# Kernel tuning notes

Hardware: AMD Instinct MI355X
Metric: run time of the kernel (lower is better)

## Reference

```python
import jax, jax.numpy as jnp
import numpy as np

SQ3, SQ5, SQ15 = 3.0**0.5, 5.0**0.5, 15.0**0.5
M0, M1, M2 = 128, 64, 32
DIM = M0 + 3*M1 + 5*M2  # 480
N_GRAPHS, ATOMS_PER, N_BLOCKS = 512, 16, 8
N_NODES = N_GRAPHS * ATOMS_PER
N_EDGES = 100000
CUTOFF = 5.0
AVG_DEGREE = 15.57
AVG_NUM_NODES = 18.03
ATOM_MAP = np.array([-1, 0, -1, -1, -1, -1, 1, 2, 3, 4], dtype=np.int32)


def _sph(u):
    # component-normalized real spherical harmonics l=1,2 of unit vectors u [E,3]
    x, y, z = u[:, 0], u[:, 1], u[:, 2]
    sh1 = SQ3 * u
    sh2 = jnp.stack([SQ15*x*y, SQ15*y*z, 0.5*SQ5*(3.0*z*z - 1.0),
                     SQ15*x*z, 0.5*SQ15*(x*x - y*y)], axis=-1)
    return sh1, sh2


def _seg_softmax(logits, seg, n):
    m = jax.ops.segment_max(logits, seg, num_segments=n)
    e = jnp.exp(logits - m[seg])
    s = jax.ops.segment_sum(e, seg, num_segments=n)
    return e / (s[seg] + 1e-9)


def _energy(pos, fp, node_atom, edge_src, edge_dst, batch):
    (atom_table, rbf_centers, rbf_width, deg_W1, deg_W2, deg_W3,
     blk_Wv0, blk_Wv1, blk_Wv2, blk_Ws0, blk_Ws1, blk_Ws2,
     blk_rW1, blk_rW2, blk_rW3, blk_Wa_src, blk_Wa_dst, blk_Wa_e, blk_wa,
     blk_ff1, blk_ff2, blk_fg1, blk_fg2, blk_fW1, blk_fW2,
     ln_g, ln_b, head_W0, head_out) = fp
    N = pos.shape[0]
    mapped = jnp.asarray(ATOM_MAP)[node_atom]
    f0 = atom_table[mapped]                       # [N,128] scalar channels
    f1 = jnp.zeros((N, M1, 3), f0.dtype)
    f2 = jnp.zeros((N, M2, 5), f0.dtype)

    vec = pos[edge_src] - pos[edge_dst]           # [E,3]
    r = jnp.sqrt(jnp.sum(vec*vec, axis=1) + 1e-12)
    u = vec / r[:, None]
    sh1, sh2 = _sph(u)
    rbf = jnp.exp(-0.5 * ((r[:, None] - rbf_centers[None, :]) / rbf_width[None, :])**2)  # [E,128]

    # edge-degree embedding: radial-weighted SH scattered to dst, scaled by avg degree
    h = jax.nn.silu(rbf @ deg_W1)
    h = jax.nn.silu(h @ deg_W2)
    g = h @ deg_W3                                 # [E,224]
    g0, g1, g2 = g[:, :M0], g[:, M0:M0+M1], g[:, M0+M1:]
    inv = 1.0 / (AVG_DEGREE ** 0.5)
    f0 = f0 + inv * jax.ops.segment_sum(g0, edge_dst, num_segments=N)
    f1 = f1 + inv * jax.ops.segment_sum(g1[:, :, None]*sh1[:, None, :], edge_dst, num_segments=N)
    f2 = f2 + inv * jax.ops.segment_sum(g2[:, :, None]*sh2[:, None, :], edge_dst, num_segments=N)

    for i in range(N_BLOCKS):
        s0, s1, s2 = f0[edge_src], f1[edge_src], f2[edge_src]
        h = jax.nn.silu(rbf @ blk_rW1[i])
        h = jax.nn.silu(h @ blk_rW2[i])
        g = h @ blk_rW3[i]
        g0, g1, g2 = g[:, :M0], g[:, M0:M0+M1], g[:, M0+M1:]
        # equivariant tensor-product messages: value path (radial-gated) + SH-injection path
        m0 = (s0 @ blk_Wv0[i]) * g0 + s0 @ blk_Ws0[i]
        m1 = jnp.einsum('ecx,cd->edx', s1, blk_Wv1[i]) * g1[:, :, None] \
             + (s0 @ blk_Ws1[i])[:, :, None] * sh1[:, None, :]
        m2 = jnp.einsum('ecx,cd->edx', s2, blk_Wv2[i]) * g2[:, :, None] \
             + (s0 @ blk_Ws2[i])[:, :, None] * sh2[:, None, :]
        # scalar attention, softmax over incoming edges per destination node
        z = jnp.tanh(s0 @ blk_Wa_src[i] + f0[edge_dst] @ blk_Wa_dst[i] + h @ blk_Wa_e[i])
        a = _seg_softmax(z @ blk_wa[i], edge_dst, N)  # [E]
        f0 = f0 + jax.ops.segment_sum(a[:, None]*m0, edge_dst, num_segments=N)
        f1 = f1 + jax.ops.segment_sum(a[:, None, None]*m1, edge_dst, num_segments=N)
        f2 = f2 + jax.ops.segment_sum(a[:, None, None]*m2, edge_dst, num_segments=N)
        # equivariant FFN: scalar MLP + scalar-gated per-l channel mixing
        f0 = f0 + jax.nn.silu(f0 @ blk_ff1[i]) @ blk_ff2[i]
        f1 = f1 + jnp.einsum('ncx,cd->ndx', f1, blk_fW1[i]) * jax.nn.sigmoid(f0 @ blk_fg1[i])[:, :, None]
        f2 = f2 + jnp.einsum('ncx,cd->ndx', f2, blk_fW2[i]) * jax.nn.sigmoid(f0 @ blk_fg2[i])[:, :, None]

    flat = jnp.concatenate([f0, f1.reshape(N, 3*M1), f2.reshape(N, 5*M2)], axis=1)  # [N,480]
    mu = jnp.mean(flat, axis=1, keepdims=True)
    var = jnp.var(flat, axis=1, keepdims=True)
    flat = (flat - mu) * jax.lax.rsqrt(var + 1e-5) * ln_g + ln_b
    # head: only the 0e part can reach the final 1x0e output (equivariance)
    e_node = jax.nn.silu(flat[:, :M0] @ head_W0) @ head_out  # [N,1]
    energy = jax.ops.segment_sum(e_node[:, 0], batch, num_segments=N_GRAPHS) / (AVG_NUM_NODES ** 0.5)
    return energy  # [B]


def setup_inputs() -> dict:
    key = jax.random.key(0)
    rng = np.random.default_rng(0)
    B, A = N_GRAPHS, ATOMS_PER
    pos_np = rng.uniform(0.0, 6.0, size=(B, A, 3)).astype(np.float32)
    d = np.linalg.norm(pos_np[:, :, None, :] - pos_np[:, None, :, :], axis=-1)
    mask = (d < CUTOFF) & (d > 1e-6)
    gi, si, di = np.nonzero(mask)
    src = np.resize((gi*A + si).astype(np.int32), N_EDGES)
    dst = np.resize((gi*A + di).astype(np.int32), N_EDGES)
    atoms = rng.choice(np.array([1, 6, 7, 8, 9], dtype=np.int32), size=B*A)
    batch = np.repeat(np.arange(B, dtype=np.int32), A)

    ks = iter(jax.random.split(key, 40))
    def W(shape, fan):
        return jax.random.normal(next(ks), shape, jnp.float32) / np.sqrt(fan)
    D3 = M0 + M1 + M2  # 224
    return dict(
        pos=jnp.asarray(pos_np.reshape(B*A, 3)),
        atom_table=W((5, M0), 1.0),
        rbf_centers=jnp.linspace(0.0, CUTOFF, 128),
        rbf_width=jnp.full((128,), 0.25, jnp.float32),
        deg_W1=W((128, 64), 128), deg_W2=W((64, 64), 64), deg_W3=W((64, D3), 64),
        blk_Wv0=W((8, M0, M0), M0), blk_Wv1=W((8, M1, M1), M1), blk_Wv2=W((8, M2, M2), M2),
        blk_Ws0=W((8, M0, M0), M0), blk_Ws1=W((8, M0, M1), M0), blk_Ws2=W((8, M0, M2), M0),
        blk_rW1=W((8, 128, 64), 128), blk_rW2=W((8, 64, 64), 64), blk_rW3=W((8, 64, D3), 64),
        blk_Wa_src=W((8, M0, 32), M0), blk_Wa_dst=W((8, M0, 32), M0), blk_Wa_e=W((8, 64, 32), 64),
        blk_wa=W((8, 32), 32),
        blk_ff1=W((8, M0, 4*M0), M0), blk_ff2=W((8, 4*M0, M0), 4*M0),
        blk_fg1=W((8, M0, M1), M0), blk_fg2=W((8, M0, M2), M0),
        blk_fW1=W((8, M1, M1), M1), blk_fW2=W((8, M2, M2), M2),
        ln_g=jnp.ones((DIM,), jnp.float32), ln_b=jnp.zeros((DIM,), jnp.float32),
        head_W0=W((M0, M0), M0), head_out=W((M0, 1), M0),
        node_atom=jnp.asarray(atoms), edge_src=jnp.asarray(src),
        edge_dst=jnp.asarray(dst), batch=jnp.asarray(batch),
    )


def reference(pos, atom_table, rbf_centers, rbf_width, deg_W1, deg_W2, deg_W3,
              blk_Wv0, blk_Wv1, blk_Wv2, blk_Ws0, blk_Ws1, blk_Ws2,
              blk_rW1, blk_rW2, blk_rW3, blk_Wa_src, blk_Wa_dst, blk_Wa_e, blk_wa,
              blk_ff1, blk_ff2, blk_fg1, blk_fg2, blk_fW1, blk_fW2,
              ln_g, ln_b, head_W0, head_out,
              node_atom, edge_src, edge_dst, batch):
    fp = (atom_table, rbf_centers, rbf_width, deg_W1, deg_W2, deg_W3,
          blk_Wv0, blk_Wv1, blk_Wv2, blk_Ws0, blk_Ws1, blk_Ws2,
          blk_rW1, blk_rW2, blk_rW3, blk_Wa_src, blk_Wa_dst, blk_Wa_e, blk_wa,
          blk_ff1, blk_ff2, blk_fg1, blk_fg2, blk_fW1, blk_fW2,
          ln_g, ln_b, head_W0, head_out)

    def _tot(p):
        e = _energy(p, fp, node_atom, edge_src, edge_dst, batch)
        return jnp.sum(e), e

    (_, energy), gpos = jax.value_and_grad(_tot, has_aux=True)(pos)
    forces = -gpos  # dy = -dE/dpos, as in the torch autograd.grad call
    return energy, forces
```

## Files before the change

### kernel.cpp

```cpp
#include <hip/hip_runtime.h>
#include <string.h>
#include <math.h>

#define NE 100000
#define NN 8192
#define NG 512
#define CHF 25000
#define NF 4
#define CHB 20000
#define NB 5
#define CHIF 50000
#define NIF 2
#define CHIB 34000
#define NIB 3
#define NNC 8192

#define SQ3F  1.7320508075688772f
#define SQ5F  2.23606797749979f
#define SQ15F 3.872983346207417f

__constant__ int c_amap[10] = {-1,0,-1,-1,-1,-1,1,2,3,4};

typedef __attribute__((ext_vector_type(4))) float f32x4;
typedef __attribute__((ext_vector_type(8))) short bf16x8;
// ... 51 lines not shown
__global__ void k_mkedge(const int* perm, const int* src, const int* dst, int* src2, int* dst2){
  int k = blockIdx.x*256 + threadIdx.x;
  if (k < NE){ int e = perm[k]; src2[k] = src[e]; dst2[k] = dst[e]; }
}

__global__ void k_wcat(const float* Wv0,const float* Ws0,const float* Ws1,const float* Ws2, float* W){
  int t = blockIdx.x*256 + threadIdx.x;
  if (t >= 8*128*352) return;
  int i = t/45056, r = t - i*45056;
  int k = r/352, n = r - k*352;
  float v;
  if (n < 128) v = Wv0[(size_t)i*16384 + k*128 + n];
  else if (n < 256) v = Ws0[(size_t)i*16384 + k*128 + (n-128)];
  else if (n < 320) v = Ws1[(size_t)i*8192 + k*64 + (n-256)];
  else v = Ws2[(size_t)i*4096 + k*32 + (n-320)];
  W[t] = v;
}

template<int MT, bool TB, bool ACC, int ACT, bool GATHER, bool SPLIT, bool ARBF, bool DMUL, bool PREOUT>
__global__ __launch_bounds__(256) void k_mgemm(
    const float* __restrict__ A, const int* __restrict__ idx,
    const float* __restrict__ B, float* __restrict__ C,
    int M, int Nd, int K,
    const float* __restrict__ cen, const float* __restrict__ wid,
    const float* __restrict__ dm, float* __restrict__ pre)
{
  constexpr int TPR = 256/MT;
  constexpr int EPT = 32/TPR;
  constexpr int RT  = MT/16;
  __shared__ unsigned short Asb[(SPLIT?2:1)*MT*40];
// ... 65 lines not shown
        if (row >= M) continue;
        size_t o = (size_t)row*Nd + col;
        float x = acc[r][v];
        if (ACC) x += C[o];
        if (DMUL) x *= dsiluf(dm[o]);
        if (PREOUT) pre[o] = x;
        if (ACT == 1) x = siluf(x);
        else if (ACT == 2) x = tanhf(x);
        else if (ACT == 3) x = sigf(x);
        C[o] = x;
      }
    }
  }
}

template<int CI, int CO, int X, bool TB, bool ACC, bool GATHER, bool SPLIT>
__global__ __launch_bounds__(256) void k_meinsum(
    const float* __restrict__ A, const int* __restrict__ idx,
    const float* __restrict__ W, float* __restrict__ C, int M)
{
  __shared__ unsigned short Asb[(SPLIT?2:1)*2560];
  __shared__ unsigned short Btb[(SPLIT?2:1)*2560];
  const int bm = blockIdx.x*64;
  const int tid = threadIdx.x, wave = tid>>6, lane = tid&63;
  const int srow = tid>>2, soff = (tid&3)*8;
  f32x4 acc[4];
  #pragma unroll
  for (int r=0;r<4;r++) acc[r] = (f32x4){0.f,0.f,0.f,0.f};
  long abase = -1;
  {
    int grow = bm + srow;
    if (grow < M*X){
      int ge = grow / X, gx = grow - ge*X;
      int ar = GATHER ? idx[ge] : ge;
// ... 33 lines not shown
      }
    }
    __syncthreads();
  }
  int col = wave*16 + (lane&15);
  if (col < CO){
    #pragma unroll
    for (int r=0;r<4;r++){
      #pragma unroll
      for (int v=0;v<4;v++){
        int row = bm + r*16 + (lane>>4)*4 + v;
        if (row >= M*X) continue;
        int ge = row / X, gx = row - ge*X;
        size_t o = (size_t)ge*CO*X + (size_t)col*X + gx;
        float xx = acc[r][v];
        if (ACC) xx += C[o];
        C[o] = xx;
      }
    }
  }
}

__global__ void k_sentinel(float* o, int n, float v){
  int i = blockIdx.x*256 + threadIdx.x;
  if (i < n) o[i] = v;
}

__global__ void k_geom(const float* __restrict__ pos, const int* __restrict__ src, const int* __restrict__ dst,
                       float* __restrict__ U, float* __restrict__ Rr, float* __restrict__ SH2b){
  int e = blockIdx.x*256 + threadIdx.x;
  if (e >= NE) return;
  int s = src[e], d = dst[e];
// ... 7 lines not shown
  SH2b[e*5+0]=SQ15F*ux*uy;
  SH2b[e*5+1]=SQ15F*uy*uz;
  SH2b[e*5+2]=0.5f*SQ5F*(3.0f*uz*uz-1.0f);
  SH2b[e*5+3]=SQ15F*ux*uz;
  SH2b[e*5+4]=0.5f*SQ15F*(ux*ux-uy*uy);
}

__global__ void k_f0init(const int* __restrict__ na, const float* __restrict__ at, float* __restrict__ f0){
  int t = blockIdx.x*256 + threadIdx.x;
  if (t >= NN*128) return;
  int n = t>>7, j = t&127;
  int m = c_amap[na[n]];
  f0[t] = at[m*128+j];
}

__global__ void k_lambda(const float* __restrict__ Z, const float* __restrict__ wa, float* __restrict__ P_c, int cnt){
  int e = blockIdx.x*256 + threadIdx.x;
  if (e >= cnt) return;
  float s = 0.0f;
  #pragma unroll
  for (int k=0;k<32;k++) s += Z[e*32+k]*wa[k];
  P_c[e] = expf(s);
}

__global__ void k_norm(const float* __restrict__ P, const float* __restrict__ S,
                       const int* __restrict__ dst, float* __restrict__ AB){
  int e = blockIdx.x*256 + threadIdx.x;
  if (e < NE) AB[e] = P[e]/(S[dst[e]]+1e-9f);
}

__global__ void k_finy(const float* __restrict__ x0,const float* __restrict__ x1,const float* __restrict__ x2,
                       float* __restrict__ y0,float* __restrict__ y1,float* __restrict__ y2,
                       const float* __restrict__ S){
  int t = blockIdx.x*256 + threadIdx.x;
  if (t >= NN*480) return;
  if (t < NN*128){ int n=t>>7; y0[t]=x0[t]+y0[t]/(S[n]+1e-9f); }
  else if (t < NN*320){ int q=t-NN*128; int n=q/192; y1[q]=x1[q]+y1[q]/(S[n]+1e-9f); }
  else { int q=t-NN*320; int n=q/160; y2[q]=x2[q]+y2[q]/(S[n]+1e-9f); }
}

__global__ void k_q3(const float* __restrict__ f0,const float* __restrict__ f1,const float* __restrict__ f2,
                     unsigned short* __restrict__ ck){
  int t = blockIdx.x*256 + threadIdx.x;
  if (t >= NN*480) return;
  float v;
  if (t < NN*128) v = f0[t];
  else if (t < NN*320) v = f1[t-NN*128];
  else v = f2[t-NN*320];
  ck[t] = f2b(v);
}
__global__ void k_dq3(const unsigned short* __restrict__ ck,
                      float* __restrict__ f0,float* __restrict__ f1,float* __restrict__ f2){
  int t = blockIdx.x*256 + threadIdx.x;
  if (t >= NN*480) return;
  float v = b2f(ck[t]);
  if (t < NN*128) f0[t]=v;
  else if (t < NN*320) f1[t-NN*128]=v;
  else f2[t-NN*320]=v;
}

template<bool INIT>
__global__ __launch_bounds__(512) void k_agg(
  float* __restrict__ f0o,float* __restrict__ f1o,float* __restrict__ f2o,
  const float* __restrict__ SC,const float* __restrict__ sv1,const float* __restrict__ sv2,
  const float* __restrict__ g,const float* __restrict__ U,const float* __restrict__ SH2b,
  const float* __restrict__ aArr,const int* __restrict__ keys,const int* __restrict__ dst,
  float* __restrict__ SACC, int c0, int c1)
{
  __shared__ float acc[7680];
  int b = blockIdx.x, lo = b<<4;
  int e0 = lbound(keys, NE, lo), e1 = lbound(keys, NE, lo+16);
  if (e0 < c0) e0 = c0;
  if (e1 > c1) e1 = c1;
// ... 171 lines not shown
      for (int x=0;x<5;x++) DSH2[e*5+x]+=c[x];
    }
    if (lane<32){
      float dsw=0.0f, dg2=0.0f;
      #pragma unroll
      for (int x=0;x<5;x++){ dsw+=dm[x]*SH2b[e*5+x]; dg2+=dm[x]*svo[x]; }
      SC[(size_t)el*352+320+lane]=dsw;
      DG[el*224+192+lane]=dg2;
      #pragma unroll
      for (int x=0;x<5;x++) SV2[el*160+lane*5+x]=dm[x]*g2;
    }
  }
}

template<int CD,int X>
__global__ void k_gatefwd(float* __restrict__ f, const float* __restrict__ V, const float* __restrict__ P){
  int t=blockIdx.x*256+threadIdx.x;
  const int ox=CD*X;
  if (t>=NN*ox) return;
  int n=t/ox, rem=t-n*ox, d=rem/X;
  f[t] += V[t]*P[n*CD+d];
}

template<int CD,int X>
__global__ void k_gateback(const float* __restrict__ dfB, float* __restrict__ V,
                           const float* __restrict__ P, float* __restrict__ DPa){
  int t=blockIdx.x*256+threadIdx.x;
  if (t>=NN*CD) return;
  float p=P[t];
  float dp=0.0f;
  #pragma unroll
  for (int x=0;x<X;x++){ dp += dfB[t*X+x]*V[t*X+x]; }
  #pragma unroll
  for (int x=0;x<X;x++){ V[t*X+x] = dfB[t*X+x]*p; }
  DPa[t] = dp*p*(1.0f-p);
}

__global__ __launch_bounds__(256) void k_dr(const float* __restrict__ DRBF, const float* __restrict__ Rr,
    const float* __restrict__ cen, const float* __restrict__ wid, float* __restrict__ DRa, int c0, int cnt){
  int w=threadIdx.x>>6, lane=threadIdx.x&63;
  int el=blockIdx.x*4+w;
  if (el>=cnt) return;
  int e=c0+el;
  float r=Rr[e], s=0.0f;
  for (int k=lane;k<128;k+=64){
    float c=cen[k], wd=wid[k];
    float t=(r-c)/wd;
    float rb=expf(-0.5f*t*t);
    s += DRBF[el*128+k]*rb*((c-r)/(wd*wd));
  }
// ... 120 lines not shown

__global__ void k_esum(const float* __restrict__ EN, float* __restrict__ out){
  int b=blockIdx.x*64+threadIdx.x;
  if (b<NG){
    float s=0.0f;
    for (int k=0;k<16;k++) s+=EN[b*16+k];
    out[b]=s;
  }
}

#define MG(MT,TB,ACC,ACT,GA,SP,AR,DM,PO, A,IDX,B,C,M,Nd,K, CEN,WID,DMp,POp) \
  k_mgemm<MT,TB,ACC,ACT,GA,SP,AR,DM,PO><<<dim3((unsigned)(((M)+(MT)-1)/(MT)),(unsigned)(((Nd)+63)/64)),dim3(256),0,stream>>>((A),(IDX),(B),(C),(M),(Nd),(K),(CEN),(WID),(DMp),(POp))
#define MGEMM(MT,TB,ACC,ACT,GA, A,IDX,B,C,M,Nd,K) MG(MT,TB,ACC,ACT,GA,false,false,false,false, A,IDX,B,C,M,Nd,K, nullptr,nullptr,nullptr,nullptr)
#define MGEMM3(MT,TB,ACC,ACT,GA, A,IDX,B,C,M,Nd,K) MG(MT,TB,ACC,ACT,GA,true,false,false,false, A,IDX,B,C,M,Nd,K, nullptr,nullptr,nullptr,nullptr)
#define MEINS(CI,CO,X,TB,ACC,GA, A,IDX,Wt,C,M) \
  k_meinsum<CI,CO,X,TB,ACC,GA,false><<<dim3((unsigned)(((M)*(X)+63)/64)),dim3(256),0,stream>>>((A),(IDX),(Wt),(C),(M))
#define MEINS3(CI,CO,X,TB,ACC,GA, A,IDX,Wt,C,M) \
  k_meinsum<CI,CO,X,TB,ACC,GA,true><<<dim3((unsigned)(((M)*(X)+63)/64)),dim3(256),0,stream>>>((A),(IDX),(Wt),(C),(M))
#define G256(n) dim3((unsigned)(((n)+255)/256)),dim3(256),0,stream
#define GW4(n) dim3((unsigned)(((n)+3)/4)),dim3(256),0,stream

extern "C" void kernel_launch(void* const* d_in, const int* in_sizes, int n_in,
                              void* d_out, int out_size, void* d_ws, size_t ws_size,
                              hipStream_t stream)
{
  const float* pos =(const float*)d_in[0];
  const float* atab=(const float*)d_in[1];
  const float* rbfc=(const float*)d_in[2];
  const float* rbfw=(const float*)d_in[3];
  const float* degW1=(const float*)d_in[4];
  const float* degW2=(const float*)d_in[5];
  const float* degW3=(const float*)d_in[6];
  const float* Wv0=(const float*)d_in[7];
// ... 27 lines not shown
  size_t off=0;
  auto al=[&](size_t n)->float*{ float* q=Wp+off; off+=n; return q; };

  const size_t SLOT = (size_t)NN*480;
  unsigned short* CKB = (unsigned short*)al((9*SLOT+1)/2);
  float* FA0=al((size_t)NN*128); float* FA1=al((size_t)NN*192); float* FA2=al((size_t)NN*160);
  float* FB0=al((size_t)NN*128); float* FB1=al((size_t)NN*192); float* FB2=al((size_t)NN*160);
  float* DI0=al((size_t)NN*128); float* DI1=al((size_t)NN*192); float* DI2=al((size_t)NN*160);
  float* DY0=al((size_t)NN*128); float* DY1=al((size_t)NN*192); float* DY2=al((size_t)NN*160);
  float* U=al((size_t)NE*3); float* Rr=al(NE); float* SH2b=al((size_t)NE*5);
  float* ABLK=al(8ULL*NE); float* LAM=al(NE);
  float* SSUM=al(NN); float* ENODE=al(NN); float* SACC=al(NN);
  float* DRr=al(NE); float* DSH1=al((size_t)NE*3); float* DSH2=al((size_t)NE*5);
  float* DPOS=al((size_t)NN*3);
  float* WCATF=al(8ULL*128*352);
  int* ROWS =(int*)al(NN+1);
  int* CNT  =(int*)al(NN);
  int* POSB =(int*)al(NN);
  int* PERMB=(int*)al(NE);
  int* ESRC2=(int*)al(NE);
  int* EDST2=(int*)al(NE);

  const size_t UNI = 28800000;
  float* UN = al(UNI);
  float* TBc=UN;
  float* DTc=TBc+(size_t)NNC*512;
  float* P1 =DTc+(size_t)NNC*512;
  float* P2 =P1 +(size_t)NN*64;
  float* V1 =P2 +(size_t)NN*32;
  float* V2 =V1 +(size_t)NN*192;
  float* DPb=V2 +(size_t)NN*160;
  float* F0N=DPb+(size_t)NN*64;

  float* outE=(float*)d_out;
  float* outF=outE+NG;

  if (off*sizeof(float) > ws_size){
    k_sentinel<<<G256(out_size)>>>(outE, out_size, (float)ws_size);
    return;
  }

  (void)hipMemsetAsync(CNT,0,NN*sizeof(int),stream);
  k_hist<<<G256(NE)>>>(edst,CNT,NE);
  k_scan0<<<dim3(1),dim3(256),0,stream>>>(CNT,ROWS);
  (void)hipMemcpyAsync(POSB,ROWS,NN*sizeof(int),hipMemcpyDeviceToDevice,stream);
  k_fillperm<<<G256(NE)>>>(edst,POSB,PERMB,NE);
  k_mkedge<<<G256(NE)>>>(PERMB,esrc,edst,ESRC2,EDST2);
  k_wcat<<<G256(8*128*352)>>>(Wv0,Ws0,Ws1,Ws2,WCATF);

  k_geom<<<G256(NE)>>>(pos,ESRC2,EDST2,U,Rr,SH2b);
  k_f0init<<<G256(NN*128)>>>(natom,atab,FA0);
  (void)hipMemsetAsync(FA1,0,(size_t)NN*192*4,stream);
  (void)hipMemsetAsync(FA2,0,(size_t)NN*160*4,stream);
  (void)hipMemsetAsync(DRr,0,(size_t)NE*4,stream);
  (void)hipMemsetAsync(DSH1,0,(size_t)NE*3*4,stream);
  (void)hipMemsetAsync(DSH2,0,(size_t)NE*5*4,stream);
  (void)hipMemsetAsync(DPOS,0,(size_t)NN*3*4,stream);

  {
    float* H1=UN; float* H2=H1+(size_t)CHIF*64; float* Gc=H2+(size_t)CHIF*64;
    for (int cc=0;cc<NIF;cc++){
      int c0e=cc*CHIF, cnt=(c0e+CHIF<=NE)?CHIF:(NE-c0e);
      MG(64,false,false,1,false, true,true,false,false, Rr+c0e,nullptr,degW1,H1, cnt,64,128, rbfc,rbfw,nullptr,nullptr);
      MGEMM3(64,false,false,1,false, H1,nullptr,degW2,H2, cnt,64,64);
      MGEMM3(64,false,false,0,false, H2,nullptr,degW3,Gc, cnt,224,64);
      k_agg<true><<<dim3(NG),dim3(512),0,stream>>>(FA0,FA1,FA2,
        nullptr,nullptr,nullptr, Gc,U,SH2b, nullptr, EDST2,EDST2, nullptr, c0e,c0e+cnt);
    }
// ... 1 lines not shown
  k_q3<<<G256(NN*480)>>>(FA0,FA1,FA2, CKB);

  float *c0_=FA0,*c1_=FA1,*c2_=FA2, *n0_=FB0,*n1_=FB1,*n2_=FB2;

  {
    float* H1  =UN;
    float* H2  =H1  +(size_t)CHF*64;
    float* Gc  =H2  +(size_t)CHF*64;
    float* SCAT=Gc  +(size_t)CHF*224;
    float* SV1 =SCAT+(size_t)CHF*352;
    float* SV2 =SV1 +(size_t)CHF*192;
    float* Zc  =SV2 +(size_t)CHF*160;
    for (int i=0;i<8;i++){
      const float* Wv1i=Wv1+(size_t)i*4096; const float* Wv2i=Wv2+(size_t)i*1024;
      const float* rW1i=rW1+(size_t)i*8192; const float* rW2i=rW2+(size_t)i*4096; const float* rW3i=rW3+(size_t)i*14336;
      const float* WaSi=WaS+(size_t)i*4096; const float* WaDi=WaD+(size_t)i*4096; const float* WaEi=WaE+(size_t)i*2048;
      const float* ff1i=ff1+(size_t)i*65536; const float* ff2i=ff2+(size_t)i*65536;
      const float* fg1i=fg1+(size_t)i*8192; const float* fg2i=fg2+(size_t)i*4096;
      const float* fW1i=fW1+(size_t)i*4096; const float* fW2i=fW2+(size_t)i*1024;
      const float* WCi=WCATF+(size_t)i*45056;
      float* AB=ABLK+(size_t)i*NE;

      (void)hipMemsetAsync(SACC,0,(size_t)NN*4,stream);
      (void)hipMemsetAsync(n0_,0,(size_t)NN*128*4,stream);
      (void)hipMemsetAsync(n1_,0,(size_t)NN*192*4,stream);
      (void)hipMemsetAsync(n2_,0,(size_t)NN*160*4,stream);
      for (int cc=0;cc<NF;cc++){
        int c0e=cc*CHF, cnt=(c0e+CHF<=NE)?CHF:(NE-c0e);
        MG(64,false,false,1,false, true,true,false,false, Rr+c0e,nullptr,rW1i,H1, cnt,64,128, rbfc,rbfw,nullptr,nullptr);
        MGEMM3(64,false,false,1,false, H1,nullptr,rW2i,H2, cnt,64,64);
        MGEMM3(64,false,false,0,false, H2,nullptr,rW3i,Gc, cnt,224,64);
        MGEMM3(64,false,false,0,true,  c0_,ESRC2+c0e,WaSi,Zc, cnt,32,128);
        MGEMM3(64,false,true, 0,true,  c0_,EDST2+c0e,WaDi,Zc, cnt,32,128);
        MGEMM3(64,false,true, 2,false, H2,nullptr,WaEi,Zc, cnt,32,64);
        k_lambda<<<G256(cnt)>>>(Zc, wab+(size_t)i*32, LAM+c0e, cnt);
        MGEMM3(64,false,false,0,true, c0_,ESRC2+c0e,WCi,SCAT, cnt,352,128);
        MEINS3(64,64,3,false,false,true, c1_,ESRC2+c0e,Wv1i,SV1, cnt);
        MEINS3(32,32,5,false,false,true, c2_,ESRC2+c0e,Wv2i,SV2, cnt);
        k_agg<false><<<dim3(NG),dim3(512),0,stream>>>(n0_,n1_,n2_,
          SCAT,SV1,SV2, Gc,U,SH2b, LAM, EDST2,EDST2, SACC, c0e,c0e+cnt);
      }
      k_norm<<<G256(NE)>>>(LAM,SACC,EDST2,AB);
      k_finy<<<G256(NN*480)>>>(c0_,c1_,c2_, n0_,n1_,n2_, SACC);
      k_q3<<<G256(NN*480)>>>(n0_,n1_,n2_, CKB+(size_t)(i+1)*SLOT);
      for (int nc=0;nc<NN/NNC;nc++){
        MGEMM3(64,false,false,1,false, n0_+(size_t)nc*NNC*128,nullptr,ff1i,TBc, NNC,512,128);
        MGEMM3(64,false,true, 0,false, TBc,nullptr,ff2i, n0_+(size_t)nc*NNC*128, NNC,128,512);
      }
      MGEMM3(32,false,false,3,false, n0_,nullptr,fg1i,P1, NN,64,128);
      MGEMM3(32,false,false,3,false, n0_,nullptr,fg2i,P2, NN,32,128);
      MEINS3(64,64,3,false,false,false, n1_,nullptr,fW1i,V1, NN);
      MEINS3(32,32,5,false,false,false, n2_,nullptr,fW2i,V2, NN);
      k_gatefwd<64,3><<<G256(NN*192)>>>(n1_,V1,P1);
      k_gatefwd<32,5><<<G256(NN*160)>>>(n2_,V2,P2);
      float* t;
      t=c0_;c0_=n0_;n0_=t; t=c1_;c1_=n1_;n1_=t; t=c2_;c2_=n2_;n2_=t;
    }
  }

  k_lnhead<<<dim3(NN),dim3(64),0,stream>>>(c0_,c1_,c2_, lng,lnb,W0h,hout, ENODE, DI0,DI1,DI2);
  k_esum<<<dim3(8),dim3(64),0,stream>>>(ENODE,outE);

  {
    float* PRE1=UN;
    float* PRE2=PRE1+(size_t)CHB*64;
    float* H1  =PRE2+(size_t)CHB*64;
    float* H2  =H1  +(size_t)CHB*64;
    float* Gc  =H2  +(size_t)CHB*64;
    float* DGc =Gc  +(size_t)CHB*224;
    float* SCAT=DGc +(size_t)CHB*224;
    float* SV1 =SCAT+(size_t)CHB*352;
    float* SV2 =SV1 +(size_t)CHB*192;
    float* Zc  =SV2 +(size_t)CHB*160;
    float* DE0 =PRE1;
    float* RBFc=DGc;
    float* DZD =Gc;
    for (int i=7;i>=0;--i){
      const float* Wv1i=Wv1+(size_t)i*4096; const float* Wv2i=Wv2+(size_t)i*1024;
      const float* rW1i=rW1+(size_t)i*8192; const float* rW2i=rW2+(size_t)i*4096; const float* rW3i=rW3+(size_t)i*14336;
      const float* WaSi=WaS+(size_t)i*4096; const float* WaDi=WaD+(size_t)i*4096; const float* WaEi=WaE+(size_t)i*2048;
      const float* ff1i=ff1+(size_t)i*65536; const float* ff2i=ff2+(size_t)i*65536;
      const float* fg1i=fg1+(size_t)i*8192; const float* fg2i=fg2+(size_t)i*4096;
      const float* fW1i=fW1+(size_t)i*4096; const float* fW2i=fW2+(size_t)i*1024;
      const float* WCi=WCATF+(size_t)i*45056;
      const float* AB=ABLK+(size_t)i*NE;

      k_dq3<<<G256(NN*480)>>>(CKB+(size_t)i*SLOT, FA0,FA1,FA2);
      if (i>0){
        const float* pf1=ff1+(size_t)(i-1)*65536; const float* pf2=ff2+(size_t)(i-1)*65536;
        const float* pg1=fg1+(size_t)(i-1)*8192; const float* pg2=fg2+(size_t)(i-1)*4096;
        const float* pW1=fW1+(size_t)(i-1)*4096; const float* pW2=fW2+(size_t)(i-1)*1024;
        for (int nc=0;nc<NN/NNC;nc++){
          MGEMM(64,false,false,1,false, FA0+(size_t)nc*NNC*128,nullptr,pf1,TBc, NNC,512,128);
          MGEMM(64,false,true, 0,false, TBc,nullptr,pf2, FA0+(size_t)nc*NNC*128, NNC,128,512);
        }
        MGEMM(32,false,false,3,false, FA0,nullptr,pg1,P1, NN,64,128);
        MGEMM(32,false,false,3,false, FA0,nullptr,pg2,P2, NN,32,128);
        MEINS(64,64,3,false,false,false, FA1,nullptr,pW1,V1, NN);
        MEINS(32,32,5,false,false,false, FA2,nullptr,pW2,V2, NN);
        k_gatefwd<64,3><<<G256(NN*192)>>>(FA1,V1,P1);
        k_gatefwd<32,5><<<G256(NN*160)>>>(FA2,V2,P2);
      }
      k_dq3<<<G256(NN*480)>>>(CKB+(size_t)(i+1)*SLOT, FB0,FB1,FB2);
      (void)hipMemcpyAsync(F0N,FB0,(size_t)NN*128*4,hipMemcpyDeviceToDevice,stream);
      for (int nc=0;nc<NN/NNC;nc++){
        MGEMM(64,false,false,1,false, FB0+(size_t)nc*NNC*128,nullptr,ff1i,TBc, NNC,512,128);
        MGEMM(64,false,true, 0,false, TBc,nullptr,ff2i, F0N+(size_t)nc*NNC*128, NNC,128,512);
      }
      MGEMM(32,false,false,3,false, F0N,nullptr,fg1i,P1, NN,64,128);
      MGEMM(32,false,false,3,false, F0N,nullptr,fg2i,P2, NN,32,128);
      MEINS(64,64,3,false,false,false, FB1,nullptr,fW1i,V1, NN);
      MEINS(32,32,5,false,false,false, FB2,nullptr,fW2i,V2, NN);
      k_gateback<64,3><<<G256(NN*64)>>>(DI1,V1,P1,DPb);
      MGEMM(64,true,true,0,false, DPb,nullptr,fg1i,DI0, NN,128,64);
      (void)hipMemcpyAsync(DY1,DI1,(size_t)NN*192*4,hipMemcpyDeviceToDevice,stream);
      MEINS(64,64,3,true,true,false, V1,nullptr,fW1i,DY1, NN);
      k_gateback<32,5><<<G256(NN*32)>>>(DI2,V2,P2,DPb);
      MGEMM(64,true,true,0,false, DPb,nullptr,fg2i,DI0, NN,128,32);
      (void)hipMemcpyAsync(DY2,DI2,(size_t)NN*160*4,hipMemcpyDeviceToDevice,stream);
      MEINS(32,32,5,true,true,false, V2,nullptr,fW2i,DY2, NN);
      (void)hipMemcpyAsync(DY0,DI0,(size_t)NN*128*4,hipMemcpyDeviceToDevice,stream);
      for (int nc=0;nc<NN/NNC;nc++){
        MGEMM(64,false,false,0,false, FB0+(size_t)nc*NNC*128,nullptr,ff1i,TBc, NNC,512,128);
        MG(64,true,false,0,false, false,false,true,false, DI0+(size_t)nc*NNC*128,nullptr,ff2i,DTc, NNC,512,128, nullptr,nullptr,TBc,nullptr);
        MGEMM(64,true,true,0,false, DTc,nullptr,ff1i, DY0+(size_t)nc*NNC*128, NNC,128,512);
      }
      k_ssum<<<dim3(NN/4),dim3(256),0,stream>>>(FA0,FA1,FA2,FB0,FB1,FB2,DY0,DY1,DY2,SSUM);
      (void)hipMemcpyAsync(DI0,DY0,(size_t)NN*128*4,hipMemcpyDeviceToDevice,stream);
      (void)hipMemcpyAsync(DI1,DY1,(size_t)NN*192*4,hipMemcpyDeviceToDevice,stream);
      (void)hipMemcpyAsync(DI2,DY2,(size_t)NN*160*4,hipMemcpyDeviceToDevice,stream);
      for (int cc=0;cc<NB;cc++){
        int c0e=cc*CHB, cnt=(c0e+CHB<=NE)?CHB:(NE-c0e);
        MG(64,false,false,1,false, false,true,false,true, Rr+c0e,nullptr,rW1i,H1, cnt,64,128, rbfc,rbfw,nullptr,PRE1);
        MG(64,false,false,1,false, false,false,false,true, H1,nullptr,rW2i,H2, cnt,64,64, nullptr,nullptr,nullptr,PRE2);
        MGEMM(64,false,false,0,false, H2,nullptr,rW3i,Gc, cnt,224,64);
        MGEMM(64,false,false,0,true,  FA0,ESRC2+c0e,WaSi,Zc, cnt,32,128);
        MGEMM(64,false,true, 0,true,  FA0,EDST2+c0e,WaDi,Zc, cnt,32,128);
        MGEMM(64,false,true, 2,false, H2,nullptr,WaEi,Zc, cnt,32,64);
        MGEMM(64,false,false,0,true, FA0,ESRC2+c0e,WCi,SCAT, cnt,352,128);
        MEINS(64,64,3,false,false,true, FA1,ESRC2+c0e,Wv1i,SV1, cnt);
        MEINS(32,32,5,false,false,true, FA2,ESRC2+c0e,Wv2i,SV2, cnt);
        k_bedge<<<GW4(cnt)>>>(SCAT,SV1,SV2, Gc,U,SH2b, DY0,DY1,DY2, EDST2, SSUM,
                              wab+(size_t)i*32, Zc, AB, DGc, DSH1, DSH2, c0e, cnt);
        MGEMM(64,true,false,0,false, Zc,nullptr,WaEi,H2, cnt,64,32);
        MG(64,true,true,0,false, false,false,true,false, DGc,nullptr,rW3i,H2, cnt,64,224, nullptr,nullptr,PRE2,nullptr);
        MG(64,true,false,0,false, false,false,true,false, H2,nullptr,rW2i,H1, cnt,64,64, nullptr,nullptr,PRE1,nullptr);
        MGEMM(64,true,false,0,false, H1,nullptr,rW1i,RBFc, cnt,128,64);
        k_dr<<<GW4(cnt)>>>(RBFc,Rr,rbfc,rbfw,DRr, c0e,cnt);
        MGEMM(64,true,false,0,false, SCAT,nullptr,WCi,DE0, cnt,128,352);
        MGEMM(64,true,true, 0,false, Zc,nullptr,WaSi,DE0, cnt,128,32);
        MGEMM(64,true,false,0,false, Zc,nullptr,WaDi,DZD, cnt,128,32);
        MEINS(64,64,3,true,false,false, SV1,nullptr,Wv1i,SV1, cnt);
        MEINS(32,32,5,true,false,false, SV2,nullptr,Wv2i,SV2, cnt);
        k_scat<<<dim3(NG),dim3(640),0,stream>>>(DI0,DI1,DI2, DE0,DZD,SV1,SV2, ESRC2,EDST2, c0e,c0e+cnt);
      }
    }
  }
// ... 27 lines not shown
```

Measured before the change: 32.96 ms.

## Fuse attention-logit GEMMs, gate GEMMs, and post-block elementwise kernels

Concatenates the src/dst/edge attention weights into one K=320 matrix so a single k_zgemm computes tanh logits and the exp(lambda) reduction in one pass. This replaces three GEMMs plus a lambda kernel, in both the forward and backward recompute. It also merges the two gate-weight GEMMs into one 96-wide GEMM and folds the gating update into the einsum epilogue. It further fuses the norm, finalize and quantize kernels, and the two dequantize kernels, into single launches. The intent is fewer launches and less intermediate memory traffic, at the cost of pointer-swapping bookkeeping between f1/f2 buffers, which could introduce aliasing mistakes.

```diff
diff --git a/kernel.cpp b/kernel.cpp
--- a/kernel.cpp
+++ b/kernel.cpp
@@ -89,6 +89,27 @@
   else if (n < 256) v = Ws0[(size_t)i*16384 + k*128 + (n-128)];
   else if (n < 320) v = Ws1[(size_t)i*8192 + k*64 + (n-256)];
   else v = Ws2[(size_t)i*4096 + k*32 + (n-320)];
+  W[t] = v;
+}
+__global__ void k_wcatz(const float* WaS,const float* WaD,const float* WaE, float* W){
+  int t = blockIdx.x*256 + threadIdx.x;
+  if (t >= 8*320*32) return;
+  int i = t/10240, r = t - i*10240;
+  int k = r/32, c = r - k*32;
+  float v;
+  if (k < 128) v = WaS[(size_t)i*4096 + k*32 + c];
+  else if (k < 256) v = WaD[(size_t)i*4096 + (k-128)*32 + c];
+  else v = WaE[(size_t)i*2048 + (k-256)*32 + c];
+  W[t] = v;
+}
+__global__ void k_wcatg(const float* fg1,const float* fg2, float* W){
+  int t = blockIdx.x*256 + threadIdx.x;
+  if (t >= 8*128*96) return;
+  int i = t/12288, r = t - i*12288;
+  int k = r/96, c = r - k*96;
+  float v;
+  if (c < 64) v = fg1[(size_t)i*8192 + k*64 + c];
+  else v = fg2[(size_t)i*4096 + k*32 + (c-64)];
   W[t] = v;
 }
 
@@ -184,10 +205,96 @@
   }
 }
 
-template<int CI, int CO, int X, bool TB, bool ACC, bool GATHER, bool SPLIT>
+template<bool SPLIT, bool LAMB>
+__global__ __launch_bounds__(256) void k_zgemm(
+    const float* __restrict__ F0, const int* __restrict__ sidx, const int* __restrict__ didx,
+    const float* __restrict__ H2v, const float* __restrict__ WZ, const float* __restrict__ wa,
+    float* __restrict__ Zc, float* __restrict__ LAM, int M)
+{
+  __shared__ unsigned short Asb[(SPLIT?2:1)*64*40];
+  __shared__ unsigned short Btb[(SPLIT?2:1)*2560];
+  __shared__ float lacc[128];
+  const int bm = blockIdx.x*64;
+  const int tid = threadIdx.x, wave = tid>>6, lane = tid&63;
+  const int arow_s = tid>>2, aoff = (tid&3)*8;
+  const int bsrow = tid>>2, bsoff = (tid&3)*8;
+  f32x4 acc[4];
+  #pragma unroll
+  for (int r=0;r<4;r++) acc[r] = (f32x4){0.f,0.f,0.f,0.f};
+  long sb=-1, db=-1, hb=-1;
+  {
+    int gr = bm + arow_s;
+    if (gr < M){ sb=(long)sidx[gr]*128; db=(long)didx[gr]*128; hb=(long)gr*64; }
+  }
+  for (int k0=0;k0<320;k0+=32){
+    long ab; int rk; const float* sp;
+    if (k0 < 128){ ab=sb; rk=k0; sp=F0; }
+    else if (k0 < 256){ ab=db; rk=k0-128; sp=F0; }
+    else { ab=hb; rk=k0-256; sp=H2v; }
+    #pragma unroll
+    for (int i=0;i<8;i++){
+      float v = (ab>=0) ? sp[ab + rk + aoff + i] : 0.0f;
+      unsigned short h = f2b(v);
+      Asb[arow_s*40 + aoff + i] = h;
+      if (SPLIT) Asb[64*40 + arow_s*40 + aoff + i] = f2b(v - b2f(h));
+    }
+    #pragma unroll
+    for (int i=0;i<8;i++){
+      int kk = k0 + bsoff + i;
+      float v = (bsrow < 32) ? WZ[kk*32 + bsrow] : 0.0f;
+      unsigned short h = f2b(v);
+      Btb[bsrow*40 + bsoff + i] = h;
+      if (SPLIT) Btb[2560 + bsrow*40 + bsoff + i] = f2b(v - b2f(h));
+    }
+    __syncthreads();
+    int boff = (wave*16 + (lane&15))*40 + (lane>>4)*8;
+    bf16x8 bh = *(const bf16x8*)&Btb[boff];
+    #pragma unroll
+    for (int r=0;r<4;r++){
+      int aoff2 = (r*16 + (lane&15))*40 + (lane>>4)*8;
+      bf16x8 ah = *(const bf16x8*)&Asb[aoff2];
+      acc[r] = __builtin_amdgcn_mfma_f32_16x16x32_bf16(ah, bh, acc[r], 0,0,0);
+      if (SPLIT){
+        bf16x8 bl = *(const bf16x8*)&Btb[2560 + boff];
+        bf16x8 al = *(const bf16x8*)&Asb[64*40 + aoff2];
+        acc[r] = __builtin_amdgcn_mfma_f32_16x16x32_bf16(ah, bl, acc[r], 0,0,0);
+        acc[r] = __builtin_amdgcn_mfma_f32_16x16x32_bf16(al, bh, acc[r], 0,0,0);
+      }
+    }
+    __syncthreads();
+  }
+  int col = wave*16 + (lane&15);
+  if (wave < 2){
+    #pragma unroll
+    for (int r=0;r<4;r++){
+      #pragma unroll
+      for (int v=0;v<4;v++){
+        int row = bm + r*16 + (lane>>4)*4 + v;
+        float z = tanhf(acc[r][v]);
+        if (row < M) Zc[(size_t)row*32 + col] = z;
+        if (LAMB){
+          float p = (row < M) ? z*wa[col] : 0.0f;
+          #pragma unroll
+          for (int o=8;o>0;o>>=1) p += __shfl_xor(p, o, 64);
+          if ((lane&15)==0) lacc[wave*64 + r*16 + (lane>>4)*4 + v] = p;
+        }
+      }
+    }
+  }
+  if (LAMB){
+    __syncthreads();
+    if (tid < 64){
+      int row = bm + tid;
+      if (row < M) LAM[row] = expf(lacc[tid] + lacc[64+tid]);
+    }
+  }
+}
+
+template<int CI, int CO, int X, bool TB, bool ACC, bool GATHER, bool SPLIT, bool GATE>
 __global__ __launch_bounds__(256) void k_meinsum(
     const float* __restrict__ A, const int* __restrict__ idx,
-    const float* __restrict__ W, float* __restrict__ C, int M)
+    const float* __restrict__ W, float* __restrict__ C, int M,
+    const float* __restrict__ P, int PS, int POFF)
 {
   __shared__ unsigned short Asb[(SPLIT?2:1)*2560];
   __shared__ unsigned short Btb[(SPLIT?2:1)*2560];
@@ -251,8 +358,13 @@
         int ge = row / X, gx = row - ge*X;
         size_t o = (size_t)ge*CO*X + (size_t)col*X + gx;
         float xx = acc[r][v];
-        if (ACC) xx += C[o];
-        C[o] = xx;
+        if (GATE){
+          float p = P[(size_t)ge*PS + POFF + col];
+          C[o] = A[o] + xx*p;
+        } else {
+          if (ACC) xx += C[o];
+          C[o] = xx;
+        }
       }
     }
   }
@@ -290,29 +402,18 @@
   f0[t] = at[m*128+j];
 }
 
-__global__ void k_lambda(const float* __restrict__ Z, const float* __restrict__ wa, float* __restrict__ P_c, int cnt){
-  int e = blockIdx.x*256 + threadIdx.x;
-  if (e >= cnt) return;
-  float s = 0.0f;
-  #pragma unroll
-  for (int k=0;k<32;k++) s += Z[e*32+k]*wa[k];
-  P_c[e] = expf(s);
-}
-
-__global__ void k_norm(const float* __restrict__ P, const float* __restrict__ S,
-                       const int* __restrict__ dst, float* __restrict__ AB){
-  int e = blockIdx.x*256 + threadIdx.x;
-  if (e < NE) AB[e] = P[e]/(S[dst[e]]+1e-9f);
-}
-
-__global__ void k_finy(const float* __restrict__ x0,const float* __restrict__ x1,const float* __restrict__ x2,
-                       float* __restrict__ y0,float* __restrict__ y1,float* __restrict__ y2,
-                       const float* __restrict__ S){
+__global__ void k_postblk(const float* __restrict__ x0,const float* __restrict__ x1,const float* __restrict__ x2,
+                          float* __restrict__ y0,float* __restrict__ y1,float* __restrict__ y2,
+                          const float* __restrict__ S, unsigned short* __restrict__ ck,
+                          const float* __restrict__ Pl, const int* __restrict__ dst, float* __restrict__ AB){
   int t = blockIdx.x*256 + threadIdx.x;
+  if (t < NE) AB[t] = Pl[t]/(S[dst[t]]+1e-9f);
   if (t >= NN*480) return;
-  if (t < NN*128){ int n=t>>7; y0[t]=x0[t]+y0[t]/(S[n]+1e-9f); }
-  else if (t < NN*320){ int q=t-NN*128; int n=q/192; y1[q]=x1[q]+y1[q]/(S[n]+1e-9f); }
-  else { int q=t-NN*320; int n=q/160; y2[q]=x2[q]+y2[q]/(S[n]+1e-9f); }
+  float v;
+  if (t < NN*128){ int n=t>>7; v = x0[t] + y0[t]/(S[n]+1e-9f); y0[t]=v; }
+  else if (t < NN*320){ int q=t-NN*128; int n=q/192; v = x1[q] + y1[q]/(S[n]+1e-9f); y1[q]=v; }
+  else { int q=t-NN*320; int n=q/160; v = x2[q] + y2[q]/(S[n]+1e-9f); y2[q]=v; }
+  ck[t] = f2b(v);
 }
 
 __global__ void k_q3(const float* __restrict__ f0,const float* __restrict__ f1,const float* __restrict__ f2,
@@ -325,14 +426,15 @@
   else v = f2[t-NN*320];
   ck[t] = f2b(v);
 }
-__global__ void k_dq3(const unsigned short* __restrict__ ck,
-                      float* __restrict__ f0,float* __restrict__ f1,float* __restrict__ f2){
+__global__ void k_dq3x2(const unsigned short* __restrict__ cka, const unsigned short* __restrict__ ckb,
+                        float* __restrict__ a0,float* __restrict__ a1,float* __restrict__ a2,
+                        float* __restrict__ b0,float* __restrict__ b1,float* __restrict__ b2){
   int t = blockIdx.x*256 + threadIdx.x;
   if (t >= NN*480) return;
-  float v = b2f(ck[t]);
-  if (t < NN*128) f0[t]=v;
-  else if (t < NN*320) f1[t-NN*128]=v;
-  else f2[t-NN*320]=v;
+  float va = b2f(cka[t]), vb = b2f(ckb[t]);
+  if (t < NN*128){ a0[t]=va; b0[t]=vb; }
+  else if (t < NN*320){ int q=t-NN*128; a1[q]=va; b1[q]=vb; }
+  else { int q=t-NN*320; a2[q]=va; b2[q]=vb; }
 }
 
 template<bool INIT>
@@ -534,26 +636,18 @@
 }
 
 template<int CD,int X>
-__global__ void k_gatefwd(float* __restrict__ f, const float* __restrict__ V, const float* __restrict__ P){
-  int t=blockIdx.x*256+threadIdx.x;
-  const int ox=CD*X;
-  if (t>=NN*ox) return;
-  int n=t/ox, rem=t-n*ox, d=rem/X;
-  f[t] += V[t]*P[n*CD+d];
-}
-
-template<int CD,int X>
 __global__ void k_gateback(const float* __restrict__ dfB, float* __restrict__ V,
-                           const float* __restrict__ P, float* __restrict__ DPa){
+                           const float* __restrict__ P12, float* __restrict__ DPa, int poff){
   int t=blockIdx.x*256+threadIdx.x;
   if (t>=NN*CD) return;
-  float p=P[t];
+  int n=t/CD, d=t-n*CD;
+  float p=P12[(size_t)n*96+poff+d];
   float dp=0.0f;
   #pragma unroll
-  for (int x=0;x<X;x++){ dp += dfB[t*X+x]*V[t*X+x]; }
+  for (int x=0;x<X;x++){ dp += dfB[(size_t)t*X+x]*V[(size_t)t*X+x]; }
   #pragma unroll
-  for (int x=0;x<X;x++){ V[t*X+x] = dfB[t*X+x]*p; }
-  DPa[t] = dp*p*(1.0f-p);
+  for (int x=0;x<X;x++){ V[(size_t)t*X+x] = dfB[(size_t)t*X+x]*p; }
+  DPa[(size_t)n*96+poff+d] = dp*p*(1.0f-p);
 }
 
 __global__ __launch_bounds__(256) void k_dr(const float* __restrict__ DRBF, const float* __restrict__ Rr,
@@ -704,9 +798,11 @@
 #define MGEMM(MT,TB,ACC,ACT,GA, A,IDX,B,C,M,Nd,K) MG(MT,TB,ACC,ACT,GA,false,false,false,false, A,IDX,B,C,M,Nd,K, nullptr,nullptr,nullptr,nullptr)
 #define MGEMM3(MT,TB,ACC,ACT,GA, A,IDX,B,C,M,Nd,K) MG(MT,TB,ACC,ACT,GA,true,false,false,false, A,IDX,B,C,M,Nd,K, nullptr,nullptr,nullptr,nullptr)
 #define MEINS(CI,CO,X,TB,ACC,GA, A,IDX,Wt,C,M) \
-  k_meinsum<CI,CO,X,TB,ACC,GA,false><<<dim3((unsigned)(((M)*(X)+63)/64)),dim3(256),0,stream>>>((A),(IDX),(Wt),(C),(M))
+  k_meinsum<CI,CO,X,TB,ACC,GA,false,false><<<dim3((unsigned)(((M)*(X)+63)/64)),dim3(256),0,stream>>>((A),(IDX),(Wt),(C),(M),nullptr,0,0)
 #define MEINS3(CI,CO,X,TB,ACC,GA, A,IDX,Wt,C,M) \
-  k_meinsum<CI,CO,X,TB,ACC,GA,true><<<dim3((unsigned)(((M)*(X)+63)/64)),dim3(256),0,stream>>>((A),(IDX),(Wt),(C),(M))
+  k_meinsum<CI,CO,X,TB,ACC,GA,true,false><<<dim3((unsigned)(((M)*(X)+63)/64)),dim3(256),0,stream>>>((A),(IDX),(Wt),(C),(M),nullptr,0,0)
+#define MEINSG(CI,CO,X,SP, A,Wt,C,M, Pp,POFF) \
+  k_meinsum<CI,CO,X,false,false,false,SP,true><<<dim3((unsigned)(((M)*(X)+63)/64)),dim3(256),0,stream>>>((A),nullptr,(Wt),(C),(M),(Pp),96,(POFF))
 #define G256(n) dim3((unsigned)(((n)+255)/256)),dim3(256),0,stream
 #define GW4(n) dim3((unsigned)(((n)+3)/4)),dim3(256),0,stream
 
@@ -764,6 +860,8 @@
   float* DRr=al(NE); float* DSH1=al((size_t)NE*3); float* DSH2=al((size_t)NE*5);
   float* DPOS=al((size_t)NN*3);
   float* WCATF=al(8ULL*128*352);
+  float* WCATZ=al(8ULL*320*32);
+  float* WCATG=al(8ULL*128*96);
   int* ROWS =(int*)al(NN+1);
   int* CNT  =(int*)al(NN);
   int* POSB =(int*)al(NN);
@@ -775,12 +873,11 @@
   float* UN = al(UNI);
   float* TBc=UN;
   float* DTc=TBc+(size_t)NNC*512;
-  float* P1 =DTc+(size_t)NNC*512;
-  float* P2 =P1 +(size_t)NN*64;
-  float* V1 =P2 +(size_t)NN*32;
+  float* P12=DTc+(size_t)NNC*512;
+  float* V1 =P12+(size_t)NN*96;
   float* V2 =V1 +(size_t)NN*192;
   float* DPb=V2 +(size_t)NN*160;
-  float* F0N=DPb+(size_t)NN*64;
+  float* F0N=DPb+(size_t)NN*96;
 
   float* outE=(float*)d_out;
   float* outF=outE+NG;
@@ -797,11 +894,12 @@
   k_fillperm<<<G256(NE)>>>(edst,POSB,PERMB,NE);
   k_mkedge<<<G256(NE)>>>(PERMB,esrc,edst,ESRC2,EDST2);
   k_wcat<<<G256(8*128*352)>>>(Wv0,Ws0,Ws1,Ws2,WCATF);
+  k_wcatz<<<G256(8*320*32)>>>(WaS,WaD,WaE,WCATZ);
+  k_wcatg<<<G256(8*128*96)>>>(fg1,fg2,WCATG);
 
   k_geom<<<G256(NE)>>>(pos,ESRC2,EDST2,U,Rr,SH2b);
   k_f0init<<<G256(NN*128)>>>(natom,atab,FA0);
-  (void)hipMemsetAsync(FA1,0,(size_t)NN*192*4,stream);
-  (void)hipMemsetAsync(FA2,0,(size_t)NN*160*4,stream);
+  (void)hipMemsetAsync(FA1,0,(size_t)NN*352*4,stream);
   (void)hipMemsetAsync(DRr,0,(size_t)NE*4,stream);
   (void)hipMemsetAsync(DSH1,0,(size_t)NE*3*4,stream);
   (void)hipMemsetAsync(DSH2,0,(size_t)NE*5*4,stream);
@@ -833,47 +931,39 @@
     for (int i=0;i<8;i++){
       const float* Wv1i=Wv1+(size_t)i*4096; const float* Wv2i=Wv2+(size_t)i*1024;
       const float* rW1i=rW1+(size_t)i*8192; const float* rW2i=rW2+(size_t)i*4096; const float* rW3i=rW3+(size_t)i*14336;
-      const float* WaSi=WaS+(size_t)i*4096; const float* WaDi=WaD+(size_t)i*4096; const float* WaEi=WaE+(size_t)i*2048;
+      const float* WZi=WCATZ+(size_t)i*10240;
       const float* ff1i=ff1+(size_t)i*65536; const float* ff2i=ff2+(size_t)i*65536;
-      const float* fg1i=fg1+(size_t)i*8192; const float* fg2i=fg2+(size_t)i*4096;
+      const float* fgCi=WCATG+(size_t)i*12288;
       const float* fW1i=fW1+(size_t)i*4096; const float* fW2i=fW2+(size_t)i*1024;
       const float* WCi=WCATF+(size_t)i*45056;
       float* AB=ABLK+(size_t)i*NE;
 
       (void)hipMemsetAsync(SACC,0,(size_t)NN*4,stream);
       (void)hipMemsetAsync(n0_,0,(size_t)NN*128*4,stream);
-      (void)hipMemsetAsync(n1_,0,(size_t)NN*192*4,stream);
-      (void)hipMemsetAsync(n2_,0,(size_t)NN*160*4,stream);
+      (void)hipMemsetAsync(n1_,0,(size_t)NN*352*4,stream);
       for (int cc=0;cc<NF;cc++){
         int c0e=cc*CHF, cnt=(c0e+CHF<=NE)?CHF:(NE-c0e);
         MG(64,false,false,1,false, true,true,false,false, Rr+c0e,nullptr,rW1i,H1, cnt,64,128, rbfc,rbfw,nullptr,nullptr);
         MGEMM3(64,false,false,1,false, H1,nullptr,rW2i,H2, cnt,64,64);
         MGEMM3(64,false,false,0,false, H2,nullptr,rW3i,Gc, cnt,224,64);
-        MGEMM3(64,false,false,0,true,  c0_,ESRC2+c0e,WaSi,Zc, cnt,32,128);
-        MGEMM3(64,false,true, 0,true,  c0_,EDST2+c0e,WaDi,Zc, cnt,32,128);
-        MGEMM3(64,false,true, 2,false, H2,nullptr,WaEi,Zc, cnt,32,64);
-        k_lambda<<<G256(cnt)>>>(Zc, wab+(size_t)i*32, LAM+c0e, cnt);
+        k_zgemm<true,true><<<dim3((unsigned)((cnt+63)/64)),dim3(256),0,stream>>>(
+            c0_, ESRC2+c0e, EDST2+c0e, H2, WZi, wab+(size_t)i*32, Zc, LAM+c0e, cnt);
         MGEMM3(64,false,false,0,true, c0_,ESRC2+c0e,WCi,SCAT, cnt,352,128);
         MEINS3(64,64,3,false,false,true, c1_,ESRC2+c0e,Wv1i,SV1, cnt);
         MEINS3(32,32,5,false,false,true, c2_,ESRC2+c0e,Wv2i,SV2, cnt);
         k_agg<false><<<dim3(NG),dim3(512),0,stream>>>(n0_,n1_,n2_,
           SCAT,SV1,SV2, Gc,U,SH2b, LAM, EDST2,EDST2, SACC, c0e,c0e+cnt);
       }
-      k_norm<<<G256(NE)>>>(LAM,SACC,EDST2,AB);
-      k_finy<<<G256(NN*480)>>>(c0_,c1_,c2_, n0_,n1_,n2_, SACC);
-      k_q3<<<G256(NN*480)>>>(n0_,n1_,n2_, CKB+(size_t)(i+1)*SLOT);
+      k_postblk<<<G256(NN*480)>>>(c0_,c1_,c2_, n0_,n1_,n2_, SACC, CKB+(size_t)(i+1)*SLOT, LAM, EDST2, AB);
       for (int nc=0;nc<NN/NNC;nc++){
         MGEMM3(64,false,false,1,false, n0_+(size_t)nc*NNC*128,nullptr,ff1i,TBc, NNC,512,128);
         MGEMM3(64,false,true, 0,false, TBc,nullptr,ff2i, n0_+(size_t)nc*NNC*128, NNC,128,512);
       }
-      MGEMM3(32,false,false,3,false, n0_,nullptr,fg1i,P1, NN,64,128);
-      MGEMM3(32,false,false,3,false, n0_,nullptr,fg2i,P2, NN,32,128);
-      MEINS3(64,64,3,false,false,false, n1_,nullptr,fW1i,V1, NN);
-      MEINS3(32,32,5,false,false,false, n2_,nullptr,fW2i,V2, NN);
-      k_gatefwd<64,3><<<G256(NN*192)>>>(n1_,V1,P1);
-      k_gatefwd<32,5><<<G256(NN*160)>>>(n2_,V2,P2);
+      MGEMM3(64,false,false,3,false, n0_,nullptr,fgCi,P12, NN,96,128);
+      MEINSG(64,64,3,true, n1_,fW1i,c1_, NN, P12, 0);
+      MEINSG(32,32,5,true, n2_,fW2i,c2_, NN, P12, 64);
       float* t;
-      t=c0_;c0_=n0_;n0_=t; t=c1_;c1_=n1_;n1_=t; t=c2_;c2_=n2_;n2_=t;
+      t=c0_;c0_=n0_;n0_=t;
     }
   }
 
@@ -897,69 +987,65 @@
     for (int i=7;i>=0;--i){
       const float* Wv1i=Wv1+(size_t)i*4096; const float* Wv2i=Wv2+(size_t)i*1024;
       const float* rW1i=rW1+(size_t)i*8192; const float* rW2i=rW2+(size_t)i*4096; const float* rW3i=rW3+(size_t)i*14336;
+      const float* WZi=WCATZ+(size_t)i*10240;
       const float* WaSi=WaS+(size_t)i*4096; const float* WaDi=WaD+(size_t)i*4096; const float* WaEi=WaE+(size_t)i*2048;
       const float* ff1i=ff1+(size_t)i*65536; const float* ff2i=ff2+(size_t)i*65536;
-      const float* fg1i=fg1+(size_t)i*8192; const float* fg2i=fg2+(size_t)i*4096;
+      const float* fgCi=WCATG+(size_t)i*12288;
       const float* fW1i=fW1+(size_t)i*4096; const float* fW2i=fW2+(size_t)i*1024;
       const float* WCi=WCATF+(size_t)i*45056;
       const float* AB=ABLK+(size_t)i*NE;
-
-      k_dq3<<<G256(NN*480)>>>(CKB+(size_t)i*SLOT, FA0,FA1,FA2);
+      float *fa1=FA1, *fa2=FA2, *dy1=DY1, *dy2=DY2;
+
+      k_dq3x2<<<G256(NN*480)>>>(CKB+(size_t)i*SLOT, CKB+(size_t)(i+1)*SLOT, FA0,FA1,FA2, FB0,FB1,FB2);
       if (i>0){
         const float* pf1=ff1+(size_t)(i-1)*65536; const float* pf2=ff2+(size_t)(i-1)*65536;
-        const float* pg1=fg1+(size_t)(i-1)*8192; const float* pg2=fg2+(size_t)(i-1)*4096;
+        const float* pgC=WCATG+(size_t)(i-1)*12288;
         const float* pW1=fW1+(size_t)(i-1)*4096; const float* pW2=fW2+(size_t)(i-1)*1024;
         for (int nc=0;nc<NN/NNC;nc++){
           MGEMM(64,false,false,1,false, FA0+(size_t)nc*NNC*128,nullptr,pf1,TBc, NNC,512,128);
           MGEMM(64,false,true, 0,false, TBc,nullptr,pf2, FA0+(size_t)nc*NNC*128, NNC,128,512);
         }
-        MGEMM(32,false,false,3,false, FA0,nullptr,pg1,P1, NN,64,128);
-        MGEMM(32,false,false,3,false, FA0,nullptr,pg2,P2, NN,32,128);
-        MEINS(64,64,3,false,false,false, FA1,nullptr,pW1,V1, NN);
-        MEINS(32,32,5,false,false,false, FA2,nullptr,pW2,V2, NN);
-        k_gatefwd<64,3><<<G256(NN*192)>>>(FA1,V1,P1);
-        k_gatefwd<32,5><<<G256(NN*160)>>>(FA2,V2,P2);
-      }
-      k_dq3<<<G256(NN*480)>>>(CKB+(size_t)(i+1)*SLOT, FB0,FB1,FB2);
+        MGEMM(64,false,false,3,false, FA0,nullptr,pgC,P12, NN,96,128);
+        MEINSG(64,64,3,false, FA1,pW1,DY1, NN, P12, 0);
+        MEINSG(32,32,5,false, FA2,pW2,DY2, NN, P12, 64);
+        fa1=DY1; dy1=FA1; fa2=DY2; dy2=FA2;
+      }
       (void)hipMemcpyAsync(F0N,FB0,(size_t)NN*128*4,hipMemcpyDeviceToDevice,stream);
       for (int nc=0;nc<NN/NNC;nc++){
         MGEMM(64,false,false,1,false, FB0+(size_t)nc*NNC*128,nullptr,ff1i,TBc, NNC,512,128);
         MGEMM(64,false,true, 0,false, TBc,nullptr,ff2i, F0N+(size_t)nc*NNC*128, NNC,128,512);
       }
-      MGEMM(32,false,false,3,false, F0N,nullptr,fg1i,P1, NN,64,128);
-      MGEMM(32,false,false,3,false, F0N,nullptr,fg2i,P2, NN,32,128);
+      MGEMM(64,false,false,3,false, F0N,nullptr,fgCi,P12, NN,96,128);
       MEINS(64,64,3,false,false,false, FB1,nullptr,fW1i,V1, NN);
       MEINS(32,32,5,false,false,false, FB2,nullptr,fW2i,V2, NN);
-      k_gateback<64,3><<<G256(NN*64)>>>(DI1,V1,P1,DPb);
-      MGEMM(64,true,true,0,false, DPb,nullptr,fg1i,DI0, NN,128,64);
-      (void)hipMemcpyAsync(DY1,DI1,(size_t)NN*192*4,hipMemcpyDeviceToDevice,stream);
-      MEINS(64,64,3,true,true,false, V1,nullptr,fW1i,DY1, NN);
-      k_gateback<32,5><<<G256(NN*32)>>>(DI2,V2,P2,DPb);
-      MGEMM(64,true,true,0,false, DPb,nullptr,fg2i,DI0, NN,128,32);
-      (void)hipMemcpyAsync(DY2,DI2,(size_t)NN*160*4,hipMemcpyDeviceToDevice,stream);
-      MEINS(32,32,5,true,true,false, V2,nullptr,fW2i,DY2, NN);
+      k_gateback<64,3><<<G256(NN*64)>>>(DI1,V1,P12,DPb,0);
+      k_gateback<32,5><<<G256(NN*32)>>>(DI2,V2,P12,DPb,64);
+      MGEMM(64,true,true,0,false, DPb,nullptr,fgCi,DI0, NN,128,96);
+      (void)hipMemcpyAsync(dy1,DI1,(size_t)NN*192*4,hipMemcpyDeviceToDevice,stream);
+      MEINS(64,64,3,true,true,false, V1,nullptr,fW1i,dy1, NN);
+      (void)hipMemcpyAsync(dy2,DI2,(size_t)NN*160*4,hipMemcpyDeviceToDevice,stream);
+      MEINS(32,32,5,true,true,false, V2,nullptr,fW2i,dy2, NN);
       (void)hipMemcpyAsync(DY0,DI0,(size_t)NN*128*4,hipMemcpyDeviceToDevice,stream);
       for (int nc=0;nc<NN/NNC;nc++){
         MGEMM(64,false,false,0,false, FB0+(size_t)nc*NNC*128,nullptr,ff1i,TBc, NNC,512,128);
         MG(64,true,false,0,false, false,false,true,false, DI0+(size_t)nc*NNC*128,nullptr,ff2i,DTc, NNC,512,128, nullptr,nullptr,TBc,nullptr);
         MGEMM(64,true,true,0,false, DTc,nullptr,ff1i, DY0+(size_t)nc*NNC*128, NNC,128,512);
       }
-      k_ssum<<<dim3(NN/4),dim3(256),0,stream>>>(FA0,FA1,FA2,FB0,FB1,FB2,DY0,DY1,DY2,SSUM);
+      k_ssum<<<dim3(NN/4),dim3(256),0,stream>>>(FA0,fa1,fa2,FB0,FB1,FB2,DY0,dy1,dy2,SSUM);
       (void)hipMemcpyAsync(DI0,DY0,(size_t)NN*128*4,hipMemcpyDeviceToDevice,stream);
-      (void)hipMemcpyAsync(DI1,DY1,(size_t)NN*192*4,hipMemcpyDeviceToDevice,stream);
-      (void)hipMemcpyAsync(DI2,DY2,(size_t)NN*160*4,hipMemcpyDeviceToDevice,stream);
+      (void)hipMemcpyAsync(DI1,dy1,(size_t)NN*192*4,hipMemcpyDeviceToDevice,stream);
+      (void)hipMemcpyAsync(DI2,dy2,(size_t)NN*160*4,hipMemcpyDeviceToDevice,stream);
       for (int cc=0;cc<NB;cc++){
         int c0e=cc*CHB, cnt=(c0e+CHB<=NE)?CHB:(NE-c0e);
         MG(64,false,false,1,false, false,true,false,true, Rr+c0e,nullptr,rW1i,H1, cnt,64,128, rbfc,rbfw,nullptr,PRE1);
         MG(64,false,false,1,false, false,false,false,true, H1,nullptr,rW2i,H2, cnt,64,64, nullptr,nullptr,nullptr,PRE2);
         MGEMM(64,false,false,0,false, H2,nullptr,rW3i,Gc, cnt,224,64);
-        MGEMM(64,false,false,0,true,  FA0,ESRC2+c0e,WaSi,Zc, cnt,32,128);
-        MGEMM(64,false,true, 0,true,  FA0,EDST2+c0e,WaDi,Zc, cnt,32,128);
-        MGEMM(64,false,true, 2,false, H2,nullptr,WaEi,Zc, cnt,32,64);
+        k_zgemm<false,false><<<dim3((unsigned)((cnt+63)/64)),dim3(256),0,stream>>>(
+            FA0, ESRC2+c0e, EDST2+c0e, H2, WZi, nullptr, Zc, nullptr, cnt);
         MGEMM(64,false,false,0,true, FA0,ESRC2+c0e,WCi,SCAT, cnt,352,128);
-        MEINS(64,64,3,false,false,true, FA1,ESRC2+c0e,Wv1i,SV1, cnt);
-        MEINS(32,32,5,false,false,true, FA2,ESRC2+c0e,Wv2i,SV2, cnt);
-        k_bedge<<<GW4(cnt)>>>(SCAT,SV1,SV2, Gc,U,SH2b, DY0,DY1,DY2, EDST2, SSUM,
+        MEINS(64,64,3,false,false,true, fa1,ESRC2+c0e,Wv1i,SV1, cnt);
+        MEINS(32,32,5,false,false,true, fa2,ESRC2+c0e,Wv2i,SV2, cnt);
+        k_bedge<<<GW4(cnt)>>>(SCAT,SV1,SV2, Gc,U,SH2b, DY0,dy1,dy2, EDST2, SSUM,
                               wab+(size_t)i*32, Zc, AB, DGc, DSH1, DSH2, c0e, cnt);
         MGEMM(64,true,false,0,false, Zc,nullptr,WaEi,H2, cnt,64,32);
         MG(64,true,true,0,false, false,false,true,false, DGc,nullptr,rW3i,H2, cnt,64,224, nullptr,nullptr,PRE2,nullptr);
```

New measurement: 31.58 ms. -4.2%, faster.
